# Optimization experiments

Hardware: AMD Instinct MI355X
Metric: run time of the kernel (lower is better)

## Reference

```python
import jax, jax.numpy as jnp
import numpy as np

N, D_IN, FC_DIM, GROUP, NONGT, EMB = 4096, 12544, 1024, 16, 300, 64
DG = FC_DIM // GROUP  # 64 per-head dim


def extract_position_matrix(bbox, nongt_dim):
    xmin, ymin, xmax, ymax = jnp.split(bbox, 4, axis=1)  # each [N,1]
    bw = xmax - xmin + 1.0
    bh = ymax - ymin + 1.0
    cx = 0.5 * (xmin + xmax)
    cy = 0.5 * (ymin + ymax)
    dx = jnp.log(jnp.maximum(jnp.abs((cx - cx.T) / bw), 1e-3))
    dy = jnp.log(jnp.maximum(jnp.abs((cy - cy.T) / bh), 1e-3))
    dw = jnp.log(bw / bw.T)
    dh = jnp.log(bh / bh.T)
    # slice to first nongt_dim columns, stack -> [N, nongt, 4]
    return jnp.stack([dx[:, :nongt_dim], dy[:, :nongt_dim],
                      dw[:, :nongt_dim], dh[:, :nongt_dim]], axis=2)


def extract_position_embedding(pos_mat, feat_dim=64, wave_length=1000.0):
    n8 = feat_dim // 8
    feat_range = jnp.arange(n8, dtype=pos_mat.dtype)
    dim_mat = wave_length ** (8.0 / feat_dim * feat_range)  # [8]
    div = 100.0 * pos_mat[..., None] / dim_mat              # [N,nongt,4,8]
    emb = jnp.concatenate([jnp.sin(div), jnp.cos(div)], axis=3)  # [N,nongt,4,16]
    return emb.reshape(pos_mat.shape[0], pos_mat.shape[1], feat_dim)


def attention_multi_head(feat, pos_emb, Wpos, bpos, Wq, bq, Wk, bk, Wo, bo):
    # feat: [N, 1024], pos_emb: [N, nongt, 64]
    nongt_feat = feat[:NONGT]                                   # [nongt, 1024]
    aff_w = jax.nn.relu(pos_emb @ Wpos + bpos)                  # [N, nongt, G]
    aff_w = jnp.swapaxes(aff_w, 1, 2)                           # [N, G, nongt]
    q = (feat @ Wq + bq).reshape(-1, GROUP, DG)                 # [N, G, dg]
    k = (nongt_feat @ Wk + bk).reshape(NONGT, GROUP, DG)        # [nongt, G, dg]
    aff = jnp.einsum('ngd,mgd->ngm', q, k) * (1.0 / np.sqrt(DG))  # [N, G, nongt]
    logits = jnp.log(jnp.maximum(aff_w, 1e-6)) + aff
    p = jax.nn.softmax(logits, axis=2)                          # [N, G, nongt]
    out = jnp.einsum('ngm,mc->ngc', p, nongt_feat)              # [N, G, 1024]
    # grouped 1x1 conv: group g maps 1024 -> 64 outputs
    lin = jnp.einsum('ngc,goc->ngo', out, Wo) + bo.reshape(GROUP, DG)
    return lin.reshape(feat.shape[0], FC_DIM)


def setup_inputs() -> dict:
    key = jax.random.key(0)
    ks = jax.random.split(key, 20)
    roi_feat = jax.random.normal(ks[0], (N, D_IN), dtype=jnp.float32)
    u = jax.random.uniform(ks[1], (N, 4), dtype=jnp.float32)
    x1 = u[:, 0:1] * 500.0
    y1 = u[:, 1:2] * 500.0
    bbox = jnp.concatenate([x1, y1, x1 + u[:, 2:3] * 200.0 + 1.0,
                            y1 + u[:, 3:4] * 200.0 + 1.0], axis=1)
    def lin(k, fin, fout):
        s = 1.0 / np.sqrt(fin)
        return jax.random.normal(k, (fin, fout), dtype=jnp.float32) * s
    inp = {'roi_feat': roi_feat, 'bbox': bbox,
           'W_fc1': lin(ks[2], D_IN, FC_DIM), 'b_fc1': jnp.zeros((FC_DIM,), jnp.float32),
           'W_fc2': lin(ks[3], FC_DIM, FC_DIM), 'b_fc2': jnp.zeros((FC_DIM,), jnp.float32)}
    for i, base in [(1, 4), (2, 10)]:
        inp[f'Wpos{i}'] = lin(ks[base], EMB, GROUP)
        inp[f'bpos{i}'] = jnp.zeros((GROUP,), jnp.float32)
        inp[f'Wq{i}'] = lin(ks[base + 1], FC_DIM, FC_DIM)
        inp[f'bq{i}'] = jnp.zeros((FC_DIM,), jnp.float32)
        inp[f'Wk{i}'] = lin(ks[base + 2], FC_DIM, FC_DIM)
        inp[f'bk{i}'] = jnp.zeros((FC_DIM,), jnp.float32)
        inp[f'Wo{i}'] = jax.random.normal(ks[base + 3], (GROUP, DG, FC_DIM), dtype=jnp.float32) * (1.0 / np.sqrt(FC_DIM))
        inp[f'bo{i}'] = jnp.zeros((FC_DIM,), jnp.float32)
    return inp


def reference(roi_feat, bbox, W_fc1, b_fc1, W_fc2, b_fc2,
              Wpos1, bpos1, Wq1, bq1, Wk1, bk1, Wo1, bo1,
              Wpos2, bpos2, Wq2, bq2, Wk2, bk2, Wo2, bo2):
    pos_mat = extract_position_matrix(bbox, NONGT)
    pos_emb = extract_position_embedding(pos_mat, EMB)
    x = roi_feat
    for (Wf, bf, Wp, bp, Wq, bq, Wk, bk, Wo, bo) in [
        (W_fc1, b_fc1, Wpos1, bpos1, Wq1, bq1, Wk1, bk1, Wo1, bo1),
        (W_fc2, b_fc2, Wpos2, bpos2, Wq2, bq2, Wk2, bk2, Wo2, bo2)]:
        x = x @ Wf + bf
        attn = attention_multi_head(x, pos_emb, Wp, bp, Wq, bq, Wk, bk, Wo, bo)
        x = jax.nn.relu(x + attn)
    return x
```

## Files before the change

### kernel.cpp

```cpp
#include <hip/hip_runtime.h>


using bf16x8 = __attribute__((ext_vector_type(8))) short;
using f32x4  = __attribute__((ext_vector_type(4))) float;
typedef unsigned short u16;
typedef unsigned int   u32;

#define DEV __device__ __forceinline__

DEV u32 cvtpk(float lo, float hi) {
  u32 r;
  asm("v_cvt_pk_bf16_f32 %0, %1, %2" : "=v"(r) : "v"(lo), "v"(hi));
  return r;
}
DEV u16 f2bf(float f) { return (u16)cvtpk(f, f); }
DEV float bf2f(u16 h) { return __uint_as_float(((u32)h) << 16); }

DEV f32x4 mfma16(bf16x8 a, bf16x8 b, f32x4 c) {
  return __builtin_amdgcn_mfma_f32_16x16x32_bf16(a, b, c, 0, 0, 0);
}
DEV void gload16(const u16* g, u16* l) {
  __builtin_amdgcn_global_load_lds((const __attribute__((address_space(1))) void*)g,
                                   (__attribute__((address_space(3))) void*)l, 16, 0, 0);
}

DEV void fsincos(float x, float* s, float* c) {
  float r = x * 0.15915494309189535f;
  r -= rintf(r);
  float a = r * 6.283185307179586f;
  *s = __sinf(a); *c = __cosf(a);
}

__constant__ float C100D[8] = {100.f, 42.16965034285822f, 17.78279410038923f,
                               7.498942093324559f, 3.1622776601683795f,
                               1.333521432163324f, 0.5623413251903491f,
                               0.23713737056616552f};

struct PrepArgs {
  const float* Wo1; u16* Wo1_b;
  const float* Wo2; u16* Wo2_b;
  const float* Wfc1; u16* Wfc1_t;
  const float* wsrc[5]; u16* wdst[5];
};

__global__ __launch_bounds__(256) void prep_kernel(PrepArgs p) {
  __shared__ float tp[32][36];
  int b = blockIdx.x, tid = threadIdx.x;
  if (b < 1024) {
    const float* src = (b < 512) ? p.Wo1 : p.Wo2;
    u16* dst = (b < 512) ? p.Wo1_b : p.Wo2_b;
    size_t i = ((size_t)(b & 511) * 256 + tid) * 8;
    float4 a = *(const float4*)(src + i);
    float4 c = *(const float4*)(src + i + 4);
    int4 v;
    v.x = (int)cvtpk(a.x, a.y); v.y = (int)cvtpk(a.z, a.w);
    v.z = (int)cvtpk(c.x, c.y); v.w = (int)cvtpk(c.z, c.w);
    *(int4*)(dst + i) = v;
    return;
  }
  const float* in; u16* out; int r0, c0, R, C;
  if (b < 13568) {
    int idx = b - 1024;
    in = p.Wfc1; out = p.Wfc1_t; R = 12544; C = 1024;
    r0 = (idx >> 5) * 32; c0 = (idx & 31) * 32;
  } else {
    int idx = b - 13568;
    int z = idx >> 10, rest = idx & 1023;
    in = p.wsrc[z]; out = p.wdst[z]; R = 1024; C = 1024;
    r0 = (rest >> 5) * 32; c0 = (rest & 31) * 32;
  }
  {
    int r = tid >> 3, c4 = (tid & 7) * 4;
    float4 v = *(const float4*)(in + (size_t)(r0 + r) * C + c0 + c4);
    *(float4*)&tp[r][c4] = v;
  }
  __syncthreads();
  {
    int c = tid >> 3, r4 = (tid & 7) * 4;
    int2 v;
    v.x = (int)cvtpk(tp[r4 + 0][c], tp[r4 + 1][c]);
    v.y = (int)cvtpk(tp[r4 + 2][c], tp[r4 + 3][c]);
    *(int2*)(out + (size_t)(c0 + c) * R + r0 + r4) = v;
  }
}

__global__ __launch_bounds__(512, 2) void gemm8p(
    const float* __restrict__ A, const u16* __restrict__ Bt,
    float* __restrict__ P) {
  const int K = 12544;
  __shared__ u16 lds[65536];
  int tid = threadIdx.x;
  int w = tid >> 6, l = tid & 63, h = l >> 4, l15 = l & 15;
  int wm = w >> 2, wn = w & 3;

  int b = ((blockIdx.x & 7) << 5) | (blockIdx.x >> 3);
  int bz = b >> 6, rest = b & 63;
  int bm = (rest & 15) * 256;
  int bn = (rest >> 4) * 256;
  size_t k0 = (size_t)bz * 3136;

  int arow = tid >> 3;
  int c0 = (tid & 7) * 8;
  const float* pA0 = A + (size_t)(bm + arow) * K + k0 + c0;
  const size_t aseg = (size_t)64 * K;
  int awe = ((arow * 128 + c0 * 2) ^ ((arow & 7) << 4)) >> 1;

  int X = ((tid >> 3) & 7) << 4;
  int lb2 = (tid * 16) ^ X;
  int lr = lb2 >> 7, lc = (lb2 & 127) >> 1;
  const u16* pB = Bt + (size_t)(bn + lr) * K + k0 + lc;
  const size_t o64 = (size_t)64 * K, o128 = (size_t)128 * K, o192 = (size_t)192 * K;

  int swz = (l15 & 7) << 3;
  int xk0 = (h * 8) ^ swz;
  int xk1 = 32 ^ xk0;
  int rA = (wm * 64 + l15) * 64;
  int rB = (wn * 32 + l15) * 64;

  f32x4 acc[8][4];
#pragma unroll
  for (int i = 0; i < 8; i++)
#pragma unroll
    for (int j = 0; j < 4; j++) acc[i][j] = (f32x4){0.f, 0.f, 0.f, 0.f};

  float4 a0[4], a1[4];
  bf16x8 af[4][2], bl[2][2], bh[2][2];

#define AISSUE(kk) { _Pragma("unroll") for (int s = 0; s < 4; s++) {     \
    a0[s] = *(const float4*)(pA0 + s * aseg + (kk));                     \
    a1[s] = *(const float4*)(pA0 + s * aseg + (kk) + 4); } }
#define BISSUE_LO(WB, kk) {                                              \
    gload16(pB + (kk),        (WB) + tid * 8);                           \
    gload16(pB + o64 + (kk),  (WB) + 4096 + tid * 8); }
#define BISSUE_HI(WB, kk) {                                              \
    gload16(pB + o128 + (kk), (WB) + 8192 + tid * 8);                    \
    gload16(pB + o192 + (kk), (WB) + 12288 + tid * 8); }
#define AWRITE(WA) { _Pragma("unroll") for (int s = 0; s < 4; s++) {     \
    int4 v;                                                              \
    v.x = (int)cvtpk(a0[s].x, a0[s].y);                                  \
    v.y = (int)cvtpk(a0[s].z, a0[s].w);                                  \
    v.z = (int)cvtpk(a1[s].x, a1[s].y);                                  \
    v.w = (int)cvtpk(a1[s].z, a1[s].w);                                  \
    *(int4*)&(WA)[awe + s * 4096] = v; } }
#define READ_AF(BASE)                                                    \
  _Pragma("unroll") for (int i = 0; i < 4; i++) {                        \
    af[i][0] = *(const bf16x8*)&LA[(BASE) + rA + i * 1024 + xk0];        \
    af[i][1] = *(const bf16x8*)&LA[(BASE) + rA + i * 1024 + xk1];        \
  }
#define READ_BL {                                                        \
  _Pragma("unroll") for (int j = 0; j < 2; j++) {                        \
    bl[j][0] = *(const bf16x8*)&LB[rB + j * 1024 + xk0];                 \
    bl[j][1] = *(const bf16x8*)&LB[rB + j * 1024 + xk1]; } }
#define READ_BH {                                                        \
  _Pragma("unroll") for (int j = 0; j < 2; j++) {                        \
    bh[j][0] = *(const bf16x8*)&LB[8192 + rB + j * 1024 + xk0];          \
    bh[j][1] = *(const bf16x8*)&LB[8192 + rB + j * 1024 + xk1]; } }
#define Q_MFMA(QR, QC, BF)                                               \
  __builtin_amdgcn_s_setprio(1);                                         \
  _Pragma("unroll") for (int i = 0; i < 4; i++)                          \
    _Pragma("unroll") for (int j = 0; j < 2; j++) {                      \
      acc[(QR)*4+i][(QC)*2+j] = mfma16(af[i][0], BF[j][0], acc[(QR)*4+i][(QC)*2+j]); \
      acc[(QR)*4+i][(QC)*2+j] = mfma16(af[i][1], BF[j][1], acc[(QR)*4+i][(QC)*2+j]); \
    }                                                                    \
  __builtin_amdgcn_s_setprio(0);
#define SBAR __builtin_amdgcn_sched_barrier(0)

  AISSUE(0);
  BISSUE_LO(lds + 16384, 0);
  BISSUE_HI(lds + 16384, 0);
  AWRITE(lds);
  asm volatile("s_waitcnt vmcnt(0) lgkmcnt(0)" ::: "memory");
  __builtin_amdgcn_s_barrier();

  for (int t = 0; t < 48; t++) {
    const u16* LA = lds + (t & 1) * 32768;
    const u16* LB = LA + 16384;
    u16* WA = lds + ((t + 1) & 1) * 32768;
    u16* WB = WA + 16384;
    int ktn = (t + 1) * 64;
    AISSUE(ktn);
    asm volatile("s_waitcnt vmcnt(10) lgkmcnt(0)" ::: "memory");
    __builtin_amdgcn_s_barrier();
    SBAR;
    READ_AF(0);
    READ_BL;
    Q_MFMA(0, 0, bl);
    SBAR;
    BISSUE_LO(WB, ktn);
    asm volatile("s_waitcnt vmcnt(10)" ::: "memory");
    __builtin_amdgcn_s_barrier();
    SBAR;
    READ_BH;
    Q_MFMA(0, 1, bh);
    SBAR;
    BISSUE_HI(WB, ktn);
    READ_AF(8192);
    Q_MFMA(1, 1, bh);
    SBAR;
    Q_MFMA(1, 0, bl);
    SBAR;
    AWRITE(WA);
  }
  {
    const u16* LA = lds;
    const u16* LB = lds + 16384;
    asm volatile("s_waitcnt vmcnt(2) lgkmcnt(0)" ::: "memory");
    __builtin_amdgcn_s_barrier();
    SBAR;
    READ_AF(0);
    READ_BL;
    Q_MFMA(0, 0, bl);
    SBAR;
    asm volatile("s_waitcnt vmcnt(0)" ::: "memory");
    __builtin_amdgcn_s_barrier();
    SBAR;
    READ_BH;
    Q_MFMA(0, 1, bh);
    SBAR;
    READ_AF(8192);
    Q_MFMA(1, 1, bh);
    Q_MFMA(1, 0, bl);
  }
#undef AISSUE
#undef BISSUE_LO
#undef BISSUE_HI
#undef AWRITE
#undef READ_AF
#undef READ_BL
#undef READ_BH
#undef Q_MFMA
#undef SBAR

  float* dst = P + (size_t)bz * 4096 * 1024;
#pragma unroll
  for (int qr = 0; qr < 2; qr++)
#pragma unroll
    for (int i = 0; i < 4; i++)
#pragma unroll
      for (int qc = 0; qc < 2; qc++)
#pragma unroll
        for (int j = 0; j < 2; j++) {
          int row0 = bm + qr * 128 + wm * 64 + i * 16 + h * 4;
          int col  = bn + qc * 128 + wn * 32 + j * 16 + l15;
          f32x4 v = acc[qr * 4 + i][qc * 2 + j];
#pragma unroll
          for (int r = 0; r < 4; r++)
            dst[(size_t)(row0 + r) * 1024 + col] = v[r];
        }
}

__global__ __launch_bounds__(256) void reduce_pos_kernel(
    const float* __restrict__ P, const float* __restrict__ bias,
    u16* __restrict__ xb,
    const float* __restrict__ bbox,
    const float* __restrict__ Wpos1, const float* __restrict__ Wpos2,
    const float* __restrict__ bpos1, const float* __restrict__ bpos2,
    u16* __restrict__ logw1, u16* __restrict__ logw2) {
  __shared__ u16 pool[18944];
  int tid = threadIdx.x;
  if (blockIdx.x < 2048) {
    const size_t MN = (size_t)4096 * 1024;
    size_t i = ((size_t)blockIdx.x * 256 + tid) * 4;
    size_t stride = (size_t)2048 * 256 * 4;
    for (; i < MN; i += stride) {
      float4 a = *(const float4*)(P + i);
      float4 b = *(const float4*)(P + MN + i);
      float4 c = *(const float4*)(P + 2 * MN + i);
      float4 d = *(const float4*)(P + 3 * MN + i);
      float4 bv = *(const float4*)(bias + (i & 1023));
      float4 r;
      r.x = a.x + b.x + c.x + d.x + bv.x;
      r.y = a.y + b.y + c.y + d.y + bv.y;
      r.z = a.z + b.z + c.z + d.z + bv.z;
      r.w = a.w + b.w + c.w + d.w + bv.w;
      int2 hv; hv.x = (int)cvtpk(r.x, r.y); hv.y = (int)cvtpk(r.z, r.w);
      *(int2*)(xb + i) = hv;
    }
    return;
  }
  u16* emb_s = pool;
  u16* wp_s  = pool + 5632;
  u16* lw_s  = pool + 8448;
  int n = blockIdx.x - 2048;
  int w = tid >> 6, l = tid & 63, h = l >> 4, l15 = l & 15;
  for (int idx = tid; idx < 1024; idx += 256) {
    int e = idx >> 4, c = idx & 15;
    wp_s[c * 88 + e]        = f2bf(Wpos1[idx]);
    wp_s[(16 + c) * 88 + e] = f2bf(Wpos2[idx]);
  }
  float4 bn = ((const float4*)bbox)[n];
  float bw_n = bn.z - bn.x + 1.f, bh_n = bn.w - bn.y + 1.f;
  float cx_n = 0.5f * (bn.x + bn.z), cy_n = 0.5f * (bn.y + bn.w);
  float bps0 = bpos1[l15], bps1 = bpos2[l15];
  int pr = tid >> 2, k = tid & 3;

  for (int m0 = 0; m0 < 320; m0 += 64) {
    int m = m0 + pr;
    float4 bm = ((const float4*)bbox)[m];
    float v;
    if (k == 0)      v = logf(fmaxf(fabsf((cx_n - 0.5f * (bm.x + bm.z)) / bw_n), 1e-3f));
    else if (k == 1) v = logf(fmaxf(fabsf((cy_n - 0.5f * (bm.y + bm.w)) / bh_n), 1e-3f));
    else if (k == 2) v = logf(bw_n / (bm.z - bm.x + 1.f));
    else             v = logf(bh_n / (bm.w - bm.y + 1.f));
    __syncthreads();
#pragma unroll
    for (int tt = 0; tt < 8; tt++) {
      float s, c; fsincos(v * C100D[tt], &s, &c);
      emb_s[pr * 88 + k * 16 + tt]     = f2bf(s);
      emb_s[pr * 88 + k * 16 + 8 + tt] = f2bf(c);
    }
    __syncthreads();
    f32x4 acc0 = {0.f, 0.f, 0.f, 0.f}, acc1 = {0.f, 0.f, 0.f, 0.f};
    bf16x8 a0 = *(const bf16x8*)&emb_s[(w * 16 + l15) * 88 + h * 8];
    bf16x8 a1 = *(const bf16x8*)&emb_s[(w * 16 + l15) * 88 + 32 + h * 8];
    bf16x8 b00 = *(const bf16x8*)&wp_s[l15 * 88 + h * 8];
    bf16x8 b01 = *(const bf16x8*)&wp_s[l15 * 88 + 32 + h * 8];
    bf16x8 b10 = *(const bf16x8*)&wp_s[(16 + l15) * 88 + h * 8];
    bf16x8 b11 = *(const bf16x8*)&wp_s[(16 + l15) * 88 + 32 + h * 8];
    acc0 = mfma16(a0, b00, acc0); acc0 = mfma16(a1, b01, acc0);
    acc1 = mfma16(a0, b10, acc1); acc1 = mfma16(a1, b11, acc1);
#pragma unroll
    for (int r = 0; r < 4; r++) {
      int mm = m0 + w * 16 + h * 4 + r;
      lw_s[l15 * 328 + mm]        = f2bf(logf(fmaxf(acc0[r] + bps0, 1e-6f)));
      lw_s[(16 + l15) * 328 + mm] = f2bf(logf(fmaxf(acc1[r] + bps1, 1e-6f)));
    }
  }
  __syncthreads();
  for (int i = tid; i < 1280; i += 256) {
    int layer = i / 640, rest = i - layer * 640;
    int gg = rest / 40, seg = rest - gg * 40;
    bf16x8 v = *(const bf16x8*)&lw_s[(layer * 16 + gg) * 328 + seg * 8];
    u16* dst = (layer ? logw2 : logw1) + ((size_t)gg * 4096 + n) * 320 + seg * 8;
    *(bf16x8*)dst = v;
  }
}

struct GDesc {
  const u16* A; const u16* Bt; const float* bias;
  u16* Cb;
  int M, N, K, ldc, nt;
};

__global__ __launch_bounds__(256, 2) void gemmU(GDesc g0, GDesc g1, GDesc g2,
                                                int c0, int c1) {
  __shared__ u16 lds[32768];
  GDesc g; int lb = blockIdx.x;
  if (lb < c0) { g = g0; lb = (lb & 7) * (c0 >> 3) + (lb >> 3); }
  else if (lb < c1) { g = g1; lb -= c0; }
  else { g = g2; lb -= c1; }
  int bm = (lb / g.nt) * 128, bn = (lb % g.nt) * 128;
  int tid = threadIdx.x;
  int w = tid >> 6, l = tid & 63, h = l >> 4, l15 = l & 15;
  int wm = w >> 1, wn = w & 1;
  int K = g.K;

  int X = ((tid >> 3) & 7) << 4;
  int lbyte = (tid * 16) ^ X;
  int lr = lbyte >> 7, lc = (lbyte & 127) >> 1;
  const u16 *pa[4], *pb[4];
#pragma unroll
  for (int c = 0; c < 4; c++) {
    pa[c] = g.A  + (size_t)min(bm + c * 32 + lr, g.M - 1) * K + lc;
    pb[c] = g.Bt + (size_t)min(bn + c * 32 + lr, g.N - 1) * K + lc;
  }

  int swz = (l15 & 7) << 3;
  int xk0 = (h * 8) ^ swz;
  int xk1 = 32 ^ xk0;
  int rA = (wm * 64 + l15) * 64;
  int rB = (wn * 64 + l15) * 64;

  f32x4 acc[4][4];
#pragma unroll
  for (int i = 0; i < 4; i++)
#pragma unroll
    for (int j = 0; j < 4; j++) acc[i][j] = (f32x4){0.f, 0.f, 0.f, 0.f};

#define ISSUEU(W, kk)                                     \
  { gload16(pa[0] + (kk), (W) + tid * 8);                 \
    gload16(pa[1] + (kk), (W) + 2048 + tid * 8);          \
    gload16(pa[2] + (kk), (W) + 4096 + tid * 8);          \
    gload16(pa[3] + (kk), (W) + 6144 + tid * 8);          \
    gload16(pb[0] + (kk), (W) + 8192 + tid * 8);          \
    gload16(pb[1] + (kk), (W) + 10240 + tid * 8);         \
    gload16(pb[2] + (kk), (W) + 12288 + tid * 8);         \
    gload16(pb[3] + (kk), (W) + 14336 + tid * 8); }

  ISSUEU(lds, 0);
  int ktiles = K >> 6;
  for (int t = 0; t < ktiles; t++) {
    const u16* LA = lds + (t & 1) * 16384;
    const u16* LB = LA + 8192;
    u16* W = lds + ((t ^ 1) & 1) * 16384;
    if (t < ktiles - 1) {
      ISSUEU(W, (t + 1) * 64);
      asm volatile("s_waitcnt vmcnt(8)" ::: "memory");
    } else {
      asm volatile("s_waitcnt vmcnt(0)" ::: "memory");
    }
    __builtin_amdgcn_s_barrier();
    asm volatile("" ::: "memory");
    bf16x8 a[4][2], bfr[4][2];
#pragma unroll
    for (int i = 0; i < 4; i++) {
      a[i][0] = *(const bf16x8*)&LA[rA + i * 1024 + xk0];
      a[i][1] = *(const bf16x8*)&LA[rA + i * 1024 + xk1];
    }
#pragma unroll
    for (int j = 0; j < 4; j++) {
      bfr[j][0] = *(const bf16x8*)&LB[rB + j * 1024 + xk0];
      bfr[j][1] = *(const bf16x8*)&LB[rB + j * 1024 + xk1];
    }
    __builtin_amdgcn_s_setprio(1);
#pragma unroll
    for (int i = 0; i < 4; i++)
#pragma unroll
      for (int j = 0; j < 4; j++) {
        acc[i][j] = mfma16(a[i][0], bfr[j][0], acc[i][j]);
        acc[i][j] = mfma16(a[i][1], bfr[j][1], acc[i][j]);
      }
    __builtin_amdgcn_s_setprio(0);
    asm volatile("" ::: "memory");
    __builtin_amdgcn_s_barrier();
  }
#undef ISSUEU

#pragma unroll
  for (int i = 0; i < 4; i++) {
#pragma unroll
    for (int j = 0; j < 4; j++) {
      int col = bn + wn * 64 + j * 16 + l15;
      if (col >= g.ldc) continue;
      float bv = (g.bias != nullptr && col < g.N) ? g.bias[col] : 0.f;
      int row0 = bm + wm * 64 + i * 16 + h * 4;
#pragma unroll
      for (int r = 0; r < 4; r++) {
        int row = row0 + r;
        if (row >= g.M) continue;
        g.Cb[(size_t)row * g.ldc + col] = f2bf(acc[i][j][r] + bv);
      }
    }
  }
}

template <bool LAST>
__global__ __launch_bounds__(256) void attn_kernel(
    const u16* __restrict__ qb, const u16* __restrict__ kb,
    const u16* __restrict__ kvt, const u16* __restrict__ logw,
    const u16* __restrict__ xr, const float* __restrict__ bo,
    float* __restrict__ outf, u16* __restrict__ outb) {
  __shared__ u16 ps[64 * 344];
  int tid = threadIdx.x;
  int g = blockIdx.y, n0 = blockIdx.x * 64;
  int w = tid >> 6, l = tid & 63, h = l >> 4, l15 = l & 15;

  {
    const u16* src = logw + ((size_t)g * 4096 + n0) * 320;
    for (int i = tid; i < 64 * 40; i += 256) {
      int row = i / 40, seg = i - row * 40;
      *(bf16x8*)&ps[row * 328 + seg * 8] = *(const bf16x8*)(src + row * 320 + seg * 8);
    }
  }
  int nrow = n0 + w * 16 + l15;
  const u16* qp = qb + (size_t)nrow * 1024 + g * 64;
  bf16x8 aq0 = *(const bf16x8*)(qp + h * 8);
  bf16x8 aq1 = *(const bf16x8*)(qp + 32 + h * 8);

  f32x4 acc[19];
#pragma unroll
  for (int f = 0; f < 19; f++) acc[f] = (f32x4){0.f, 0.f, 0.f, 0.f};
  const u16* kp = kb + g * 64 + h * 8;
#pragma unroll
  for (int f = 0; f < 19; f++) {
    bf16x8 b0 = *(const bf16x8*)(kp + (size_t)(f * 16 + l15) * 1024);
    bf16x8 b1 = *(const bf16x8*)(kp + (size_t)(f * 16 + l15) * 1024 + 32);
    acc[f] = mfma16(aq0, b0, acc[f]);
    acc[f] = mfma16(aq1, b1, acc[f]);
  }
  __syncthreads();

  int nbase = n0 + w * 16 + h * 4;
  int lrow = w * 16 + h * 4;
  float mx[4] = {-INFINITY, -INFINITY, -INFINITY, -INFINITY};
  float sm[4] = {0.f, 0.f, 0.f, 0.f};
#pragma unroll
  for (int f = 0; f < 19; f++) {
    int m = f * 16 + l15;
#pragma unroll
    for (int r = 0; r < 4; r++) {
      float lw = -INFINITY;
      if (m < 300) lw = bf2f(ps[(lrow + r) * 328 + m]);
      float lg = acc[f][r] * 0.125f + lw;
      acc[f][r] = lg;
      mx[r] = fmaxf(mx[r], lg);
    }
  }
#pragma unroll
  for (int d = 1; d < 16; d <<= 1)
#pragma unroll
    for (int r = 0; r < 4; r++) mx[r] = fmaxf(mx[r], __shfl_xor(mx[r], d));
#pragma unroll
  for (int f = 0; f < 19; f++)
#pragma unroll
    for (int r = 0; r < 4; r++) {
      float p = __expf(acc[f][r] - mx[r]);
      acc[f][r] = p; sm[r] += p;
    }
#pragma unroll
  for (int d = 1; d < 16; d <<= 1)
#pragma unroll
    for (int r = 0; r < 4; r++) sm[r] += __shfl_xor(sm[r], d);
  float inv[4];
#pragma unroll
  for (int r = 0; r < 4; r++) inv[r] = 1.f / sm[r];

  __syncthreads();
#pragma unroll
  for (int f = 0; f < 19; f++)
#pragma unroll
    for (int r = 0; r < 4; r++)
      ps[(lrow + r) * 344 + f * 16 + l15] = f2bf(acc[f][r]);
#pragma unroll
  for (int r = 0; r < 4; r++)
    ps[(lrow + r) * 344 + 304 + l15] = 0;

  f32x4 acc2[4];
#pragma unroll
  for (int fo = 0; fo < 4; fo++) acc2[fo] = (f32x4){0.f, 0.f, 0.f, 0.f};
  const u16* vp = kvt + (size_t)g * 64 * 320 + h * 8;
#pragma unroll
  for (int ks = 0; ks < 10; ks++) {
    bf16x8 ap = *(const bf16x8*)&ps[(w * 16 + l15) * 344 + ks * 32 + h * 8];
#pragma unroll
    for (int fo = 0; fo < 4; fo++) {
      bf16x8 bv = *(const bf16x8*)(vp + (size_t)(fo * 16 + l15) * 320 + ks * 32);
      acc2[fo] = mfma16(ap, bv, acc2[fo]);
    }
  }
#pragma unroll
  for (int fo = 0; fo < 4; fo++) {
    int col = g * 64 + fo * 16 + l15;
    float bov = bo[col];
#pragma unroll
    for (int r = 0; r < 4; r++) {
      int row = nbase + r;
      size_t off = (size_t)row * 1024 + col;
      float v = bf2f(xr[off]) + acc2[fo][r] * inv[r] + bov;
      v = fmaxf(v, 0.f);
      if (LAST) outf[off] = v;
      else      outb[off] = f2bf(v);
    }
  }
}

extern "C" void kernel_launch(void* const* d_in, const int* in_sizes, int n_in,
                              void* d_out, int out_size, void* d_ws, size_t ws_size,
                              hipStream_t stream) {
  (void)in_sizes; (void)n_in; (void)out_size; (void)ws_size;
  const float* roi   = (const float*)d_in[0];
  const float* bbox  = (const float*)d_in[1];
  const float* Wfc1  = (const float*)d_in[2];
  const float* bfc1  = (const float*)d_in[3];
  const float* Wfc2  = (const float*)d_in[4];
  const float* bfc2  = (const float*)d_in[5];
  const float* Wpos1 = (const float*)d_in[6];
  const float* bpos1 = (const float*)d_in[7];
  const float* Wq1   = (const float*)d_in[8];
  const float* bq1   = (const float*)d_in[9];
  const float* Wk1   = (const float*)d_in[10];
  const float* bk1   = (const float*)d_in[11];
  const float* Wo1   = (const float*)d_in[12];
  const float* bo1   = (const float*)d_in[13];
  const float* Wpos2 = (const float*)d_in[14];
  const float* bpos2 = (const float*)d_in[15];
  const float* Wq2   = (const float*)d_in[16];
  const float* bq2   = (const float*)d_in[17];
  const float* Wk2   = (const float*)d_in[18];
  const float* bk2   = (const float*)d_in[19];
  const float* Wo2   = (const float*)d_in[20];
  const float* bo2   = (const float*)d_in[21];

  char* ws = (char*)d_ws;
  u16*  Wfc1_t = (u16*)(ws + 102760448);
  u16*  Wfc2_t = (u16*)(ws + 128450560);
  u16*  Wq1_t  = (u16*)(ws + 130547712);
  u16*  Wk1_t  = (u16*)(ws + 132644864);
  u16*  Wq2_t  = (u16*)(ws + 134742016);
  u16*  Wk2_t  = (u16*)(ws + 136839168);
  u16*  Wo1_b  = (u16*)(ws + 138936320);
  u16*  Wo2_b  = (u16*)(ws + 141033472);
  float* Pp    = (float*)(ws + 143134720);
  u16*  xb_f   = (u16*)(ws + 243798016);
  u16*  xb_a   = (u16*)(ws + 252186624);
  u16*  q_b    = (u16*)(ws + 260575232);
  u16*  k_b    = (u16*)(ws + 268963840);
  u16*  kvt_b  = (u16*)(ws + 269578240);
  u16*  logw1  = (u16*)(ws + 270233600);
  u16*  logw2  = (u16*)(ws + 312176640);

  {
    PrepArgs p;
    p.Wo1 = Wo1;   p.Wo1_b = Wo1_b;
    p.Wo2 = Wo2;   p.Wo2_b = Wo2_b;
    p.Wfc1 = Wfc1; p.Wfc1_t = Wfc1_t;
    p.wsrc[0] = Wfc2; p.wdst[0] = Wfc2_t;
    p.wsrc[1] = Wq1;  p.wdst[1] = Wq1_t;
    p.wsrc[2] = Wk1;  p.wdst[2] = Wk1_t;
    p.wsrc[3] = Wq2;  p.wdst[3] = Wq2_t;
    p.wsrc[4] = Wk2;  p.wdst[4] = Wk2_t;
    prep_kernel<<<18688, 256, 0, stream>>>(p);
  }
  gemm8p<<<256, 512, 0, stream>>>(roi, Wfc1_t, Pp);
  reduce_pos_kernel<<<6144, 256, 0, stream>>>(Pp, bfc1, xb_f, bbox,
                                              Wpos1, Wpos2, bpos1, bpos2,
                                              logw1, logw2);
  {
    GDesc q  = {xb_f,  Wq1_t, bq1, q_b,   4096, 1024, 1024, 1024, 8};
    GDesc kk = {xb_f,  Wk1_t, bk1, k_b,    300, 1024, 1024, 1024, 8};
    GDesc kv = {Wo1_b, xb_f,  nullptr, kvt_b, 1024, 300, 1024, 320, 3};
    gemmU<<<304, 256, 0, stream>>>(q, kk, kv, 256, 280);
  }
  attn_kernel<false><<<dim3(64, 16), 256, 0, stream>>>(q_b, k_b, kvt_b, logw1, xb_f, bo1, nullptr, xb_a);

  {
    GDesc fc = {xb_a, Wfc2_t, bfc2, xb_f, 4096, 1024, 1024, 1024, 8};
    gemmU<<<256, 256, 0, stream>>>(fc, fc, fc, 256, 256);
  }
  {
    GDesc q  = {xb_f,  Wq2_t, bq2, q_b,   4096, 1024, 1024, 1024, 8};
    GDesc kk = {xb_f,  Wk2_t, bk2, k_b,    300, 1024, 1024, 1024, 8};
    GDesc kv = {Wo2_b, xb_f,  nullptr, kvt_b, 1024, 300, 1024, 320, 3};
    gemmU<<<304, 256, 0, stream>>>(q, kk, kv, 256, 280);
  }
  attn_kernel<true><<<dim3(64, 16), 256, 0, stream>>>(q_b, k_b, kvt_b, logw2, xb_f, bo2, (float*)d_out, nullptr);
}
```

Before: 383.3 us.

## Restructure fc1 split-K GEMM into BK=32 triple-buffered LDS pipeline

The fp32-A/bf16-B split-K GEMM main loop now uses a K-step of 32 instead of 64, with three LDS stages of 16K elements instead of two stages of 32K. A is prefetched two steps ahead into alternating register sets, and B is loaded two stages ahead via direct global-to-LDS loads. Each step has one barrier instead of two, and the LDS swizzle is rebuilt for 64-byte rows. The aim is deeper prefetch and less LDS per block, in exchange for twice as many loop iterations and barriers per K range, and a new swizzle that may cause bank conflicts.

Result: slower. 397.4 us (+3.7%).

```diff
diff --git a/kernel.cpp b/kernel.cpp
--- a/kernel.cpp
+++ b/kernel.cpp
@@ -88,7 +88,7 @@
     const float* __restrict__ A, const u16* __restrict__ Bt,
     float* __restrict__ P) {
   const int K = 12544;
-  __shared__ u16 lds[65536];
+  __shared__ u16 lds[49152];
   int tid = threadIdx.x;
   int w = tid >> 6, l = tid & 63, h = l >> 4, l15 = l & 15;
   int wm = w >> 2, wn = w & 3;
@@ -99,23 +99,25 @@
   int bn = (rest >> 4) * 256;
   size_t k0 = (size_t)bz * 3136;
 
-  int arow = tid >> 3;
-  int c0 = (tid & 7) * 8;
-  const float* pA0 = A + (size_t)(bm + arow) * K + k0 + c0;
-  const size_t aseg = (size_t)64 * K;
-  int awe = ((arow * 128 + c0 * 2) ^ ((arow & 7) << 4)) >> 1;
-
-  int X = ((tid >> 3) & 7) << 4;
-  int lb2 = (tid * 16) ^ X;
-  int lr = lb2 >> 7, lc = (lb2 & 127) >> 1;
-  const u16* pB = Bt + (size_t)(bn + lr) * K + k0 + lc;
-  const size_t o64 = (size_t)64 * K, o128 = (size_t)128 * K, o192 = (size_t)192 * K;
-
-  int swz = (l15 & 7) << 3;
-  int xk0 = (h * 8) ^ swz;
-  int xk1 = 32 ^ xk0;
-  int rA = (wm * 64 + l15) * 64;
-  int rB = (wn * 32 + l15) * 64;
+  int arw = tid >> 1, acl = (tid & 1) * 16;
+  const float* pA0 = A + (size_t)(bm + arw) * K + k0 + acl;
+  int aswz = ((arw >> 1) & 3) << 4;
+  int awq0 = ((arw * 64 + acl * 2)      ^ aswz) >> 1;
+  int awq1 = ((arw * 64 + acl * 2 + 16) ^ aswz) >> 1;
+
+  const u16* pBg0; const u16* pBg1;
+  {
+    int d0 = tid * 16, d1 = 8192 + tid * 16;
+    int r0 = d0 >> 6, r1 = d1 >> 6;
+    int s0 = ((d0 & 63) ^ (((r0 >> 1) & 3) << 4)) >> 1;
+    int s1 = ((d1 & 63) ^ (((r1 >> 1) & 3) << 4)) >> 1;
+    pBg0 = Bt + (size_t)(bn + r0) * K + k0 + s0;
+    pBg1 = Bt + (size_t)(bn + r1) * K + k0 + s1;
+  }
+
+  int xk = (h * 8) ^ (((l15 >> 1) & 3) << 3);
+  int rA = (wm * 64 + l15) * 32;
+  int rB = (wn * 32 + l15) * 32;
 
   f32x4 acc[8][4];
 #pragma unroll
@@ -123,112 +125,88 @@
 #pragma unroll
     for (int j = 0; j < 4; j++) acc[i][j] = (f32x4){0.f, 0.f, 0.f, 0.f};
 
-  float4 a0[4], a1[4];
-  bf16x8 af[4][2], bl[2][2], bh[2][2];
-
-#define AISSUE(kk) { _Pragma("unroll") for (int s = 0; s < 4; s++) {     \
-    a0[s] = *(const float4*)(pA0 + s * aseg + (kk));                     \
-    a1[s] = *(const float4*)(pA0 + s * aseg + (kk) + 4); } }
-#define BISSUE_LO(WB, kk) {                                              \
-    gload16(pB + (kk),        (WB) + tid * 8);                           \
-    gload16(pB + o64 + (kk),  (WB) + 4096 + tid * 8); }
-#define BISSUE_HI(WB, kk) {                                              \
-    gload16(pB + o128 + (kk), (WB) + 8192 + tid * 8);                    \
-    gload16(pB + o192 + (kk), (WB) + 12288 + tid * 8); }
-#define AWRITE(WA) { _Pragma("unroll") for (int s = 0; s < 4; s++) {     \
-    int4 v;                                                              \
-    v.x = (int)cvtpk(a0[s].x, a0[s].y);                                  \
-    v.y = (int)cvtpk(a0[s].z, a0[s].w);                                  \
-    v.z = (int)cvtpk(a1[s].x, a1[s].y);                                  \
-    v.w = (int)cvtpk(a1[s].z, a1[s].w);                                  \
-    *(int4*)&(WA)[awe + s * 4096] = v; } }
-#define READ_AF(BASE)                                                    \
-  _Pragma("unroll") for (int i = 0; i < 4; i++) {                        \
-    af[i][0] = *(const bf16x8*)&LA[(BASE) + rA + i * 1024 + xk0];        \
-    af[i][1] = *(const bf16x8*)&LA[(BASE) + rA + i * 1024 + xk1];        \
-  }
-#define READ_BL {                                                        \
-  _Pragma("unroll") for (int j = 0; j < 2; j++) {                        \
-    bl[j][0] = *(const bf16x8*)&LB[rB + j * 1024 + xk0];                 \
-    bl[j][1] = *(const bf16x8*)&LB[rB + j * 1024 + xk1]; } }
-#define READ_BH {                                                        \
-  _Pragma("unroll") for (int j = 0; j < 2; j++) {                        \
-    bh[j][0] = *(const bf16x8*)&LB[8192 + rB + j * 1024 + xk0];          \
-    bh[j][1] = *(const bf16x8*)&LB[8192 + rB + j * 1024 + xk1]; } }
-#define Q_MFMA(QR, QC, BF)                                               \
-  __builtin_amdgcn_s_setprio(1);                                         \
-  _Pragma("unroll") for (int i = 0; i < 4; i++)                          \
+  float4 s0r[4], s1r[4];
+
+#define AISSUE(R, kk) { R[0] = *(const float4*)(pA0 + (kk));             \
+    R[1] = *(const float4*)(pA0 + (kk) + 4);                             \
+    R[2] = *(const float4*)(pA0 + (kk) + 8);                             \
+    R[3] = *(const float4*)(pA0 + (kk) + 12); }
+#define AWRITE(R, BUF) {                                                 \
+    int4 v0, v1;                                                         \
+    v0.x = (int)cvtpk(R[0].x, R[0].y); v0.y = (int)cvtpk(R[0].z, R[0].w);\
+    v0.z = (int)cvtpk(R[1].x, R[1].y); v0.w = (int)cvtpk(R[1].z, R[1].w);\
+    v1.x = (int)cvtpk(R[2].x, R[2].y); v1.y = (int)cvtpk(R[2].z, R[2].w);\
+    v1.z = (int)cvtpk(R[3].x, R[3].y); v1.w = (int)cvtpk(R[3].z, R[3].w);\
+    *(int4*)&lds[(BUF) + awq0] = v0;                                     \
+    *(int4*)&lds[(BUF) + awq1] = v1; }
+#define BISSUE(BUF, kk) {                                                \
+    gload16(pBg0 + (kk), &lds[(BUF) + 8192 + tid * 8]);                  \
+    gload16(pBg1 + (kk), &lds[(BUF) + 12288 + tid * 8]); }
+#define SBAR __builtin_amdgcn_sched_barrier(0)
+#define MFMA_PHASE(BUF) {                                                \
+    const u16* LA = lds + (BUF); const u16* LB = LA + 8192;              \
+    bf16x8 bl[2], bh[2], af[4];                                          \
     _Pragma("unroll") for (int j = 0; j < 2; j++) {                      \
-      acc[(QR)*4+i][(QC)*2+j] = mfma16(af[i][0], BF[j][0], acc[(QR)*4+i][(QC)*2+j]); \
-      acc[(QR)*4+i][(QC)*2+j] = mfma16(af[i][1], BF[j][1], acc[(QR)*4+i][(QC)*2+j]); \
+      bl[j] = *(const bf16x8*)&LB[rB + j * 512 + xk];                    \
+      bh[j] = *(const bf16x8*)&LB[4096 + rB + j * 512 + xk];             \
     }                                                                    \
-  __builtin_amdgcn_s_setprio(0);
-#define SBAR __builtin_amdgcn_sched_barrier(0)
-
-  AISSUE(0);
-  BISSUE_LO(lds + 16384, 0);
-  BISSUE_HI(lds + 16384, 0);
-  AWRITE(lds);
+    _Pragma("unroll") for (int i = 0; i < 4; i++)                        \
+      af[i] = *(const bf16x8*)&LA[rA + i * 512 + xk];                    \
+    __builtin_amdgcn_s_setprio(1);                                       \
+    _Pragma("unroll") for (int i = 0; i < 4; i++)                        \
+      _Pragma("unroll") for (int j = 0; j < 2; j++) {                    \
+        acc[i][j]     = mfma16(af[i], bl[j], acc[i][j]);                 \
+        acc[i][2 + j] = mfma16(af[i], bh[j], acc[i][2 + j]);             \
+      }                                                                  \
+    __builtin_amdgcn_s_setprio(0);                                       \
+    SBAR;                                                                \
+    _Pragma("unroll") for (int i = 0; i < 4; i++)                        \
+      af[i] = *(const bf16x8*)&LA[4096 + rA + i * 512 + xk];             \
+    __builtin_amdgcn_s_setprio(1);                                       \
+    _Pragma("unroll") for (int i = 0; i < 4; i++)                        \
+      _Pragma("unroll") for (int j = 0; j < 2; j++) {                    \
+        acc[4 + i][j]     = mfma16(af[i], bl[j], acc[4 + i][j]);         \
+        acc[4 + i][2 + j] = mfma16(af[i], bh[j], acc[4 + i][2 + j]);     \
+      }                                                                  \
+    __builtin_amdgcn_s_setprio(0); }
+#define ITER(T, RW, RL) {                                                \
+    AISSUE(RL, ((T) + 2) * 32);                                          \
+    asm volatile("s_waitcnt vmcnt(10) lgkmcnt(0)" ::: "memory");         \
+    __builtin_amdgcn_s_barrier();                                        \
+    SBAR;                                                                \
+    BISSUE(nx2, ((T) + 2) * 32);                                         \
+    MFMA_PHASE(cub);                                                     \
+    SBAR;                                                                \
+    AWRITE(RW, nx1);                                                     \
+    cub = nx1; nx1 = nx2; nx2 = (nx2 == 32768) ? 0 : nx2 + 16384; }
+
+  AISSUE(s0r, 0);
+  BISSUE(0, 0);
+  AWRITE(s0r, 0);
+  AISSUE(s1r, 32);
+  BISSUE(16384, 32);
+  int cub = 0, nx1 = 16384, nx2 = 32768;
+
+  for (int tt = 0; tt < 48; tt++) {
+    ITER(2 * tt,     s1r, s0r);
+    ITER(2 * tt + 1, s0r, s1r);
+  }
+  asm volatile("s_waitcnt vmcnt(6) lgkmcnt(0)" ::: "memory");
+  __builtin_amdgcn_s_barrier();
+  SBAR;
+  MFMA_PHASE(cub);
+  SBAR;
+  AWRITE(s1r, nx1);
+  cub = nx1;
   asm volatile("s_waitcnt vmcnt(0) lgkmcnt(0)" ::: "memory");
   __builtin_amdgcn_s_barrier();
-
-  for (int t = 0; t < 48; t++) {
-    const u16* LA = lds + (t & 1) * 32768;
-    const u16* LB = LA + 16384;
-    u16* WA = lds + ((t + 1) & 1) * 32768;
-    u16* WB = WA + 16384;
-    int ktn = (t + 1) * 64;
-    AISSUE(ktn);
-    asm volatile("s_waitcnt vmcnt(10) lgkmcnt(0)" ::: "memory");
-    __builtin_amdgcn_s_barrier();
-    SBAR;
-    READ_AF(0);
-    READ_BL;
-    Q_MFMA(0, 0, bl);
-    SBAR;
-    BISSUE_LO(WB, ktn);
-    asm volatile("s_waitcnt vmcnt(10)" ::: "memory");
-    __builtin_amdgcn_s_barrier();
-    SBAR;
-    READ_BH;
-    Q_MFMA(0, 1, bh);
-    SBAR;
-    BISSUE_HI(WB, ktn);
-    READ_AF(8192);
-    Q_MFMA(1, 1, bh);
-    SBAR;
-    Q_MFMA(1, 0, bl);
-    SBAR;
-    AWRITE(WA);
-  }
-  {
-    const u16* LA = lds;
-    const u16* LB = lds + 16384;
-    asm volatile("s_waitcnt vmcnt(2) lgkmcnt(0)" ::: "memory");
-    __builtin_amdgcn_s_barrier();
-    SBAR;
-    READ_AF(0);
-    READ_BL;
-    Q_MFMA(0, 0, bl);
-    SBAR;
-    asm volatile("s_waitcnt vmcnt(0)" ::: "memory");
-    __builtin_amdgcn_s_barrier();
-    SBAR;
-    READ_BH;
-    Q_MFMA(0, 1, bh);
-    SBAR;
-    READ_AF(8192);
-    Q_MFMA(1, 1, bh);
-    Q_MFMA(1, 0, bl);
-  }
+  SBAR;
+  MFMA_PHASE(cub);
 #undef AISSUE
-#undef BISSUE_LO
-#undef BISSUE_HI
 #undef AWRITE
-#undef READ_AF
-#undef READ_BL
-#undef READ_BH
-#undef Q_MFMA
+#undef BISSUE
+#undef MFMA_PHASE
+#undef ITER
 #undef SBAR
 
   float* dst = P + (size_t)bz * 4096 * 1024;
```
